# Kernel optimization log

Hardware: AMD Instinct MI355X
Metric: run time of the kernel (lower is better)

Reference implementation:

```python
import jax, jax.numpy as jnp
import numpy as np

B, S, D = 1, 2048, 4096
H = 32
Q_RANK, KV_RANK = 1536, 512
NOPE, ROPE, VD = 128, 64, 128
QD = NOPE + ROPE  # 192
EPS = 1e-6
THETA = 10000.0


def setup_inputs() -> dict:
    key = jax.random.key(0)
    ks = jax.random.split(key, 8)
    std = 0.02
    return {
        'hidden_states': jax.random.normal(ks[0], (B, S, D), jnp.float32),
        'Wq_a': jax.random.normal(ks[1], (D, Q_RANK), jnp.float32) * std,
        'q_a_ln_w': jnp.ones((Q_RANK,), jnp.float32),
        'Wq_b': jax.random.normal(ks[2], (Q_RANK, H * QD), jnp.float32) * std,
        'Wkv_a': jax.random.normal(ks[3], (D, KV_RANK + ROPE), jnp.float32) * std,
        'kv_a_ln_w': jnp.ones((KV_RANK,), jnp.float32),
        'Wkv_b': jax.random.normal(ks[4], (KV_RANK, H * (NOPE + VD)), jnp.float32) * std,
        'Wo': jax.random.normal(ks[5], (H * VD, D), jnp.float32) * std,
    }


def _rmsnorm(x, w):
    return x * jax.lax.rsqrt(jnp.mean(x * x, axis=-1, keepdims=True) + EPS) * w


def _rotate_half(x):
    h = x.shape[-1] // 2
    return jnp.concatenate([-x[..., h:], x[..., :h]], axis=-1)


def _apply_rope(x, cos, sin):
    # DeepSeek interleave permutation: view(..., d//2, 2).transpose -> [evens | odds]
    xp = jnp.concatenate([x[..., 0::2], x[..., 1::2]], axis=-1)
    return xp * cos + _rotate_half(xp) * sin


def _mla_forward(hidden_states, Wq_a, q_a_ln_w, Wq_b, Wkv_a, kv_a_ln_w, Wkv_b, Wo):
    b, s, _ = hidden_states.shape
    # low-rank query projection
    q = _rmsnorm(hidden_states @ Wq_a, q_a_ln_w) @ Wq_b          # [b,s,H*QD]
    q = q.reshape(b, s, H, QD).transpose(0, 2, 1, 3)             # [b,H,s,QD]
    q_nope, q_pe = q[..., :NOPE], q[..., NOPE:]
    # compressed kv + shared rope key
    ckv = hidden_states @ Wkv_a                                   # [b,s,KV_RANK+ROPE]
    compressed, k_pe = ckv[..., :KV_RANK], ckv[..., KV_RANK:]
    kv = _rmsnorm(compressed, kv_a_ln_w) @ Wkv_b                 # [b,s,H*(NOPE+VD)]
    kv = kv.reshape(b, s, H, NOPE + VD).transpose(0, 2, 1, 3)    # [b,H,s,NOPE+VD]
    k_nope, v = kv[..., :NOPE], kv[..., NOPE:]
    k_pe = k_pe[:, None, :, :]                                    # [b,1,s,ROPE]
    # rotary tables (cos/sin duplicated halves)
    inv_freq = 1.0 / (THETA ** (jnp.arange(0, ROPE, 2, dtype=jnp.float32) / ROPE))
    freqs = jnp.outer(jnp.arange(s, dtype=jnp.float32), inv_freq)  # [s,ROPE/2]
    emb = jnp.concatenate([freqs, freqs], axis=-1)                 # [s,ROPE]
    cos = jnp.cos(emb)[None, None].astype(hidden_states.dtype)
    sin = jnp.sin(emb)[None, None].astype(hidden_states.dtype)
    q_pe = _apply_rope(q_pe, cos, sin)
    k_pe = _apply_rope(k_pe, cos, sin)
    # assemble full q/k heads
    qf = jnp.concatenate([q_nope, q_pe], axis=-1)                 # [b,H,s,QD]
    kf = jnp.concatenate([k_nope, jnp.broadcast_to(k_pe, (b, H, s, ROPE))], axis=-1)
    scale = QD ** (-0.5)
    scores = jnp.einsum('bhqd,bhkd->bhqk', qf, kf) * scale        # [b,H,s,s]
    causal = jnp.tril(jnp.ones((s, s), dtype=bool))
    scores = jnp.where(causal, scores, jnp.finfo(scores.dtype).min)
    probs = jax.nn.softmax(scores, axis=-1)
    o = jnp.einsum('bhqk,bhkd->bhqd', probs, v)                   # [b,H,s,VD]
    o = o.transpose(0, 2, 1, 3).reshape(b, s, H * VD)
    return o @ Wo


def reference(hidden_states, Wq_a, q_a_ln_w, Wq_b, Wkv_a, kv_a_ln_w, Wkv_b, Wo):
    return _mla_forward(hidden_states, Wq_a, q_a_ln_w, Wq_b, Wkv_a, kv_a_ln_w, Wkv_b, Wo)
```

## Files before the change

### kernel.cpp

```cpp
#include <hip/hip_runtime.h>

typedef unsigned short u16;
using bf16x8 = __attribute__((ext_vector_type(8))) __bf16;
using f32x4  = __attribute__((ext_vector_type(4))) float;
using s16x8  = __attribute__((ext_vector_type(8))) short;
using s16x4  = __attribute__((ext_vector_type(4))) short;

#define AS1 __attribute__((address_space(1)))
#define AS3 __attribute__((address_space(3)))

__device__ __forceinline__ void gload16(const u16* g, u16* l) {
  __builtin_amdgcn_global_load_lds((AS1 void*)(size_t)g, (AS3 void*)l, 16, 0, 0);
}

__device__ __forceinline__ u16 f2bf(float f) {
  unsigned u = __float_as_uint(f);
  u += 0x7fffu + ((u >> 16) & 1u);
  return (u16)(u >> 16);
}
__device__ __forceinline__ float bf2f(u16 h) {
  return __uint_as_float(((unsigned)h) << 16);
}

__global__ __launch_bounds__(256) void cast_bf16_kernel(const float* __restrict__ x,
                                                        u16* __restrict__ y, int n) {
  int i = (blockIdx.x * 256 + threadIdx.x) * 4;
  if (i + 3 < n) {
    float4 v = *reinterpret_cast<const float4*>(x + i);
    s16x4 o;
    o[0] = (short)f2bf(v.x); o[1] = (short)f2bf(v.y);
    o[2] = (short)f2bf(v.z); o[3] = (short)f2bf(v.w);
    *reinterpret_cast<s16x4*>(y + i) = o;
  }
}

__global__ __launch_bounds__(256) void transpose_cast_kernel(const float* __restrict__ W,
                                                             u16* __restrict__ WT,
                                                             int K, int N) {
  __shared__ u16 tile[64][72];
  const int t = threadIdx.x;
  const int nb = blockIdx.x * 64, kb = blockIdx.y * 64;
  const int rr = t >> 3;
  const int cc = (t & 7) * 8;
#pragma unroll
  for (int pass = 0; pass < 2; ++pass) {
    const float* src = W + (size_t)(kb + pass * 32 + rr) * N + nb + cc;
    float4 a = *reinterpret_cast<const float4*>(src);
    float4 b = *reinterpret_cast<const float4*>(src + 4);
    u16* tr = &tile[pass * 32 + rr][cc];
    tr[0] = f2bf(a.x); tr[1] = f2bf(a.y); tr[2] = f2bf(a.z); tr[3] = f2bf(a.w);
    tr[4] = f2bf(b.x); tr[5] = f2bf(b.y); tr[6] = f2bf(b.z); tr[7] = f2bf(b.w);
  }
  __syncthreads();
#pragma unroll
  for (int pass = 0; pass < 2; ++pass) {
    s16x8 v;
#pragma unroll
    for (int j = 0; j < 8; ++j) v[j] = (short)tile[cc + j][pass * 32 + rr];
    *reinterpret_cast<s16x8*>(WT + (size_t)(nb + pass * 32 + rr) * K + kb + cc) = v;
  }
}

__global__ __launch_bounds__(256) void rmsnorm_kernel(const u16* __restrict__ x,
                                                      const float* __restrict__ w,
                                                      u16* __restrict__ y,
                                                      int R, int xs, int ys) {
  const int row = blockIdx.x, t = threadIdx.x;
  const u16* xr = x + (size_t)row * xs;
  float ss = 0.f;
  for (int i = t; i < R; i += 256) { float f = bf2f(xr[i]); ss += f * f; }
#pragma unroll
  for (int m = 32; m >= 1; m >>= 1) ss += __shfl_xor(ss, m);
  __shared__ float red[4];
  if ((t & 63) == 0) red[t >> 6] = ss;
  __syncthreads();
  float tot = red[0] + red[1] + red[2] + red[3];
  float r = rsqrtf(tot / (float)R + 1e-6f);
  u16* yr = y + (size_t)row * ys;
  for (int i = t; i < R; i += 256) yr[i] = f2bf(bf2f(xr[i]) * r * w[i]);
}

__global__ __launch_bounds__(256) void rope_table_kernel(float* __restrict__ cost,
                                                         float* __restrict__ sint) {
  int idx = blockIdx.x * 256 + threadIdx.x;
  int pos = idx >> 5, j = idx & 31;
  float inv = __expf(-(float)j * (9.210340371976184f / 32.0f));
  float f = (float)pos * inv;
  cost[idx] = cosf(f);
  sint[idx] = sinf(f);
}

__global__ __launch_bounds__(256) void build_qf_kernel(const u16* __restrict__ q,
                                                       const float* __restrict__ cost,
                                                       const float* __restrict__ sint,
                                                       u16* __restrict__ qf) {
  int tid = blockIdx.x * 256 + threadIdx.x;
  int o8 = tid * 8;
  if (o8 >= 32 * 2048 * 192) return;
  const float scale = 0.07216878364870323f;
  int c = (o8 % 192) >> 3;
  int rest = o8 / 192;
  int s = rest & 2047, h = rest >> 11;
  const u16* qrow = q + ((size_t)s * 32 + h) * 192;
  s16x8 out;
  if (c < 16) {
    s16x8 v = *reinterpret_cast<const s16x8*>(qrow + c * 8);
#pragma unroll
    for (int j = 0; j < 8; ++j) out[j] = (short)f2bf(bf2f((u16)v[j]) * scale);
  } else {
    int j0 = c * 8 - 128;
    bool lo = j0 < 32;
    int jj0 = lo ? j0 : j0 - 32;
    s16x8 a = *reinterpret_cast<const s16x8*>(qrow + 128 + 2 * jj0);
    s16x8 b = *reinterpret_cast<const s16x8*>(qrow + 128 + 2 * jj0 + 8);
    float4 c0 = *reinterpret_cast<const float4*>(cost + s * 32 + jj0);
    float4 c1 = *reinterpret_cast<const float4*>(cost + s * 32 + jj0 + 4);
    float4 s0 = *reinterpret_cast<const float4*>(sint + s * 32 + jj0);
    float4 s1 = *reinterpret_cast<const float4*>(sint + s * 32 + jj0 + 4);
    float cs[8] = {c0.x, c0.y, c0.z, c0.w, c1.x, c1.y, c1.z, c1.w};
    float sn[8] = {s0.x, s0.y, s0.z, s0.w, s1.x, s1.y, s1.z, s1.w};
#pragma unroll
    for (int j = 0; j < 8; ++j) {
      float x0 = bf2f((u16)((j < 4) ? a[2 * j] : b[2 * j - 8]));
      float x1 = bf2f((u16)((j < 4) ? a[2 * j + 1] : b[2 * j - 7]));
      float v = lo ? (x0 * cs[j] - x1 * sn[j]) : (x1 * cs[j] + x0 * sn[j]);
      out[j] = (short)f2bf(v * scale);
    }
  }
  *reinterpret_cast<s16x8*>(qf + o8) = out;
}

__global__ __launch_bounds__(256) void build_kf_kernel(const u16* __restrict__ kv,
                                                       const u16* __restrict__ ckv,
                                                       const float* __restrict__ cost,
                                                       const float* __restrict__ sint,
                                                       u16* __restrict__ kf) {
  int tid = blockIdx.x * 256 + threadIdx.x;
  int o8 = tid * 8;
  if (o8 >= 32 * 2048 * 192) return;
  int c = (o8 % 192) >> 3;
  int rest = o8 / 192;
  int s = rest & 2047, h = rest >> 11;
  s16x8 out;
  if (c < 16) {
    out = *reinterpret_cast<const s16x8*>(kv + ((size_t)s * 32 + h) * 256 + c * 8);
  } else {
    int j0 = c * 8 - 128;
    bool lo = j0 < 32;
    int jj0 = lo ? j0 : j0 - 32;
    const u16* crow = ckv + (size_t)s * 2112 + 512;
    s16x8 a = *reinterpret_cast<const s16x8*>(crow + 2 * jj0);
    s16x8 b = *reinterpret_cast<const s16x8*>(crow + 2 * jj0 + 8);
    float4 c0 = *reinterpret_cast<const float4*>(cost + s * 32 + jj0);
    float4 c1 = *reinterpret_cast<const float4*>(cost + s * 32 + jj0 + 4);
    float4 s0 = *reinterpret_cast<const float4*>(sint + s * 32 + jj0);
    float4 s1 = *reinterpret_cast<const float4*>(sint + s * 32 + jj0 + 4);
    float cs[8] = {c0.x, c0.y, c0.z, c0.w, c1.x, c1.y, c1.z, c1.w};
    float sn[8] = {s0.x, s0.y, s0.z, s0.w, s1.x, s1.y, s1.z, s1.w};
#pragma unroll
    for (int j = 0; j < 8; ++j) {
      float x0 = bf2f((u16)((j < 4) ? a[2 * j] : b[2 * j - 8]));
      float x1 = bf2f((u16)((j < 4) ? a[2 * j + 1] : b[2 * j - 7]));
      float v = lo ? (x0 * cs[j] - x1 * sn[j]) : (x1 * cs[j] + x0 * sn[j]);
      out[j] = (short)f2bf(v);
    }
  }
  *reinterpret_cast<s16x8*>(kf + o8) = out;
}

__global__ __launch_bounds__(256) void vt_build_kernel(const u16* __restrict__ kv,
                                                       u16* __restrict__ vT) {
  __shared__ u16 tile[64][72];
  const int t = threadIdx.x;
  const int sb = blockIdx.x * 64, db = blockIdx.y * 64, h = blockIdx.z;
  const int rr = t >> 3, cc = (t & 7) * 8;
#pragma unroll
  for (int pass = 0; pass < 2; ++pass) {
    const u16* src = kv + (size_t)(sb + pass * 32 + rr) * 8192 + h * 256 + 128 + db + cc;
    s16x8 v = *reinterpret_cast<const s16x8*>(src);
#pragma unroll
    for (int j = 0; j < 8; ++j) tile[pass * 32 + rr][cc + j] = (u16)v[j];
  }
  __syncthreads();
#pragma unroll
  for (int pass = 0; pass < 2; ++pass) {
    s16x8 v;
#pragma unroll
    for (int j = 0; j < 8; ++j) v[j] = (short)tile[cc + j][pass * 32 + rr];
    *reinterpret_cast<s16x8*>(vT + ((size_t)h * 128 + db + pass * 32 + rr) * 2048 + sb + cc) = v;
  }
}

template <int OUT_BF16>
__global__ __launch_bounds__(256) void gemm_v3_kernel(const u16* __restrict__ A,
                                                      const u16* __restrict__ BT,
                                                      void* __restrict__ Cv,
                                                      int M, int N, int K) {
  __shared__ __align__(16) u16 S[4 * 8192];
  const int t0 = threadIdx.x;
  const int lane = t0 & 63, wave = t0 >> 6;
  const int wr = wave >> 1, wc = wave & 1;
  const int row0 = blockIdx.y * 128, col0 = blockIdx.x * 128;
  const int lrow = lane & 15, lkg = lane >> 4;

  const int lp = lane ^ ((lane >> 3) & 3);
  const int srow_off = lp >> 2;
  const int skel = (lp & 3) * 8;
  const int c0 = wave * 2, c1 = c0 + 1;
  const int arow_c0 = row0 + c0 * 16 + srow_off;
  const int arow_c1 = row0 + c1 * 16 + srow_off;
  int brow_c0 = col0 + c0 * 16 + srow_off; if (brow_c0 > N - 1) brow_c0 = N - 1;
  int brow_c1 = col0 + c1 * 16 + srow_off; if (brow_c1 > N - 1) brow_c1 = N - 1;

  int aoff[4], boff[4];
#pragma unroll
  for (int m = 0; m < 4; ++m) {
    int r = wr * 64 + m * 16 + lrow;
    int off = r * 32 + lkg * 8;
    aoff[m] = off ^ ((off >> 3) & 0x18);
    r = wc * 64 + m * 16 + lrow;
    off = r * 32 + lkg * 8;
    boff[m] = off ^ ((off >> 3) & 0x18);
  }

  const int NT = K >> 5;

#pragma unroll
  for (int pt = 0; pt < 3; ++pt) {
    u16* ab = &S[pt * 8192];
    const int kb = pt * 32 + skel;
    gload16(A  + (size_t)arow_c0 * K + kb, ab + c0 * 512);
    gload16(A  + (size_t)arow_c1 * K + kb, ab + c1 * 512);
    gload16(BT + (size_t)brow_c0 * K + kb, ab + 4096 + c0 * 512);
    gload16(BT + (size_t)brow_c1 * K + kb, ab + 4096 + c1 * 512);
  }

  f32x4 acc[4][4];
#pragma unroll
  for (int m = 0; m < 4; ++m)
#pragma unroll
    for (int n = 0; n < 4; ++n) acc[m][n] = 0.f;

  for (int t = 0; t < NT; ++t) {
    if (t + 2 < NT)      asm volatile("s_waitcnt vmcnt(8)" ::: "memory");
    else if (t + 1 < NT) asm volatile("s_waitcnt vmcnt(4)" ::: "memory");
    else                 asm volatile("s_waitcnt vmcnt(0)" ::: "memory");
    __builtin_amdgcn_s_barrier();
    __builtin_amdgcn_sched_barrier(0);

    const u16* ab = &S[(t & 3) * 8192];
    bf16x8 af[4], bb[4];
#pragma unroll
    for (int m = 0; m < 4; ++m)
      af[m] = *reinterpret_cast<const bf16x8*>(ab + aoff[m]);
#pragma unroll
    for (int n = 0; n < 4; ++n)
      bb[n] = *reinterpret_cast<const bf16x8*>(ab + 4096 + boff[n]);

    if (t + 3 < NT) {
      u16* sb = &S[((t + 3) & 3) * 8192];
      const int kb = (t + 3) * 32 + skel;
      gload16(A  + (size_t)arow_c0 * K + kb, sb + c0 * 512);
      gload16(A  + (size_t)arow_c1 * K + kb, sb + c1 * 512);
      gload16(BT + (size_t)brow_c0 * K + kb, sb + 4096 + c0 * 512);
      gload16(BT + (size_t)brow_c1 * K + kb, sb + 4096 + c1 * 512);
    }

    __builtin_amdgcn_s_setprio(1);
#pragma unroll
    for (int m = 0; m < 4; ++m)
#pragma unroll
      for (int n = 0; n < 4; ++n)
        acc[m][n] = __builtin_amdgcn_mfma_f32_16x16x32_bf16(af[m], bb[n], acc[m][n], 0, 0, 0);
    __builtin_amdgcn_s_setprio(0);
  }

#pragma unroll
  for (int m = 0; m < 4; ++m) {
#pragma unroll
    for (int n = 0; n < 4; ++n) {
      int col = col0 + wc * 64 + n * 16 + lrow;
      if (col < N) {
#pragma unroll
        for (int i = 0; i < 4; ++i) {
          int row = row0 + wr * 64 + m * 16 + lkg * 4 + i;
          size_t idx = (size_t)row * N + col;
          if (OUT_BF16) ((u16*)Cv)[idx] = f2bf(acc[m][n][i]);
          else          ((float*)Cv)[idx] = acc[m][n][i];
        }
      }
    }
  }
}

__global__ __launch_bounds__(256) void mla_attn_kernel(const u16* __restrict__ qf,
                                                       const u16* __restrict__ kf,
                                                       const u16* __restrict__ vT,
                                                       u16* __restrict__ o) {
  const int h = blockIdx.x, pair = blockIdx.y;
  const int t = threadIdx.x, wave = t >> 6, lane = t & 63;
  const int lrow = lane & 15, lkg = lane >> 4;
  __shared__ __align__(16) u16 Kt[24 * 512];
  __shared__ __align__(16) u16 Vt[16 * 512];
  __shared__ __align__(16) u16 Pl[4][16][72];

  const u16* ksrc0 = kf + ((size_t)h * 2048 + wave * 16 + lrow) * 192 + lkg * 8;
  const u16* vsrc0 = vT + ((size_t)h * 128 + wave * 32 + lrow) * 2048 + lkg * 8;

  for (int qq = 0; qq < 2; ++qq) {
    const int qb = qq ? (31 - pair) : pair;
    const int qbase = qb * 64 + wave * 16;

    bf16x8 qfr[6];
    const u16* qrow_ptr = qf + ((size_t)h * 2048 + qbase + lrow) * 192;
#pragma unroll
    for (int kk = 0; kk < 6; ++kk)
      qfr[kk] = *reinterpret_cast<const bf16x8*>(qrow_ptr + kk * 32 + lkg * 8);

    f32x4 acc_o[8];
#pragma unroll
    for (int f = 0; f < 8; ++f) acc_o[f] = 0.f;
    float m_run[4], l_run[4];
#pragma unroll
    for (int i = 0; i < 4; ++i) { m_run[i] = -__builtin_inff(); l_run[i] = 0.f; }

    const int kv_end = qb * 64 + 64;
    for (int kt = 0; kt < kv_end; kt += 64) {
      {
        const u16* ks = ksrc0 + (size_t)kt * 192;
#pragma unroll
        for (int kk = 0; kk < 6; ++kk)
          gload16(ks + kk * 32, &Kt[(wave * 6 + kk) * 512]);
#pragma unroll
        for (int j = 0; j < 4; ++j) {
          int fo = (j >> 1), ck = j & 1;
          gload16(vsrc0 + (size_t)fo * 16 * 2048 + kt + ck * 32,
                  &Vt[((wave * 2 + fo) * 2 + ck) * 512]);
        }
      }
      __syncthreads();

      f32x4 sv[4];
#pragma unroll
      for (int cg = 0; cg < 4; ++cg) sv[cg] = 0.f;
#pragma unroll
      for (int cg = 0; cg < 4; ++cg)
#pragma unroll
        for (int kk = 0; kk < 6; ++kk) {
          bf16x8 kfr = *reinterpret_cast<const bf16x8*>(&Kt[(cg * 6 + kk) * 512 + lane * 8]);
          sv[cg] = __builtin_amdgcn_mfma_f32_16x16x32_bf16(qfr[kk], kfr, sv[cg], 0, 0, 0);
        }

      const int qrow_b = qbase + lkg * 4;
      if (kt + 64 >= kv_end) {
#pragma unroll
        for (int cg = 0; cg < 4; ++cg) {
          int kvcol = kt + cg * 16 + lrow;
#pragma unroll
          for (int i = 0; i < 4; ++i)
            if (kvcol > qrow_b + i) sv[cg][i] = -__builtin_inff();
        }
      }
      float tmax[4], m_new[4], alpha[4], rsum[4], p[4][4];
#pragma unroll
      for (int i = 0; i < 4; ++i)
        tmax[i] = fmaxf(fmaxf(sv[0][i], sv[1][i]), fmaxf(sv[2][i], sv[3][i]));
#pragma unroll
      for (int m = 8; m >= 1; m >>= 1)
#pragma unroll
        for (int i = 0; i < 4; ++i) tmax[i] = fmaxf(tmax[i], __shfl_xor(tmax[i], m));
#pragma unroll
      for (int i = 0; i < 4; ++i) {
        m_new[i] = fmaxf(m_run[i], tmax[i]);
#pragma unroll
        for (int cg = 0; cg < 4; ++cg) p[cg][i] = __expf(sv[cg][i] - m_new[i]);
        rsum[i] = (p[0][i] + p[1][i]) + (p[2][i] + p[3][i]);
      }
#pragma unroll
      for (int m = 8; m >= 1; m >>= 1)
#pragma unroll
        for (int i = 0; i < 4; ++i) rsum[i] += __shfl_xor(rsum[i], m);
#pragma unroll
      for (int i = 0; i < 4; ++i) {
        alpha[i] = __expf(m_run[i] - m_new[i]);
        l_run[i] = l_run[i] * alpha[i] + rsum[i];
        m_run[i] = m_new[i];
      }
#pragma unroll
      for (int f = 0; f < 8; ++f)
#pragma unroll
        for (int i = 0; i < 4; ++i) acc_o[f][i] *= alpha[i];
#pragma unroll
      for (int cg = 0; cg < 4; ++cg)
#pragma unroll
        for (int i = 0; i < 4; ++i)
          Pl[wave][lkg * 4 + i][cg * 16 + lrow] = f2bf(p[cg][i]);
#pragma unroll
      for (int ck = 0; ck < 2; ++ck) {
        bf16x8 pf = *reinterpret_cast<const bf16x8*>(&Pl[wave][lrow][ck * 32 + lkg * 8]);
#pragma unroll
        for (int f = 0; f < 8; ++f) {
          bf16x8 vfr = *reinterpret_cast<const bf16x8*>(&Vt[(f * 2 + ck) * 512 + lane * 8]);
          acc_o[f] = __builtin_amdgcn_mfma_f32_16x16x32_bf16(pf, vfr, acc_o[f], 0, 0, 0);
        }
      }
      __syncthreads();
    }
#pragma unroll
    for (int f = 0; f < 8; ++f)
#pragma unroll
      for (int i = 0; i < 4; ++i) {
        int row = qbase + lkg * 4 + i;
        int col = h * 128 + f * 16 + lrow;
        o[(size_t)row * 4096 + col] = f2bf(acc_o[f][i] / l_run[i]);
      }
  }
}

extern "C" void kernel_launch(void* const* d_in, const int* in_sizes, int n_in,
                              void* d_out, int out_size, void* d_ws, size_t ws_size,
                              hipStream_t stream) {
  (void)in_sizes; (void)n_in; (void)out_size; (void)ws_size;
  const float* hs   = (const float*)d_in[0];
  const float* Wqa  = (const float*)d_in[1];
  const float* qln  = (const float*)d_in[2];
  const float* Wqb  = (const float*)d_in[3];
  const float* Wkva = (const float*)d_in[4];
  const float* kvln = (const float*)d_in[5];
  const float* Wkvb = (const float*)d_in[6];
  const float* Wo   = (const float*)d_in[7];
  float* out = (float*)d_out;

  char* p = (char*)d_ws;
  size_t off = 0;
  auto carve = [&](size_t bytes) {
    char* r = p + off;
    off += (bytes + 255) & ~(size_t)255;
    return r;
  };
  u16* hs_bf = (u16*)carve((size_t)2048 * 4096 * 2);
  u16* WabT  = (u16*)carve((size_t)2112 * 4096 * 2);
  u16* WqbT  = (u16*)carve((size_t)6144 * 1536 * 2);
  u16* WkvbT = (u16*)carve((size_t)8192 * 512 * 2);
  u16* WoT   = (u16*)carve((size_t)4096 * 4096 * 2);
  u16* fused = (u16*)carve((size_t)2048 * 2112 * 2);
  u16* qan   = (u16*)carve((size_t)2048 * 1536 * 2);
  u16* q     = (u16*)carve((size_t)2048 * 6144 * 2);
  u16* cn    = (u16*)carve((size_t)2048 * 512 * 2);
  u16* kv    = (u16*)carve((size_t)2048 * 8192 * 2);
  u16* qfb   = (u16*)carve((size_t)32 * 2048 * 192 * 2);
  u16* kfb   = (u16*)carve((size_t)32 * 2048 * 192 * 2);
  u16* vTb   = (u16*)carve((size_t)32 * 128 * 2048 * 2);
  u16* ob    = (u16*)carve((size_t)2048 * 4096 * 2);
  float* cost = (float*)carve((size_t)65536 * 4);
  float* sint = (float*)carve((size_t)65536 * 4);

  cast_bf16_kernel<<<8192, 256, 0, stream>>>(hs, hs_bf, 2048 * 4096);
  transpose_cast_kernel<<<dim3(24, 64), 256, 0, stream>>>(Wqa, WabT, 4096, 1536);
  transpose_cast_kernel<<<dim3(9, 64), 256, 0, stream>>>(Wkva, WabT + (size_t)1536 * 4096, 4096, 576);
  transpose_cast_kernel<<<dim3(96, 24), 256, 0, stream>>>(Wqb, WqbT, 1536, 6144);
  transpose_cast_kernel<<<dim3(128, 8), 256, 0, stream>>>(Wkvb, WkvbT, 512, 8192);
  transpose_cast_kernel<<<dim3(64, 64), 256, 0, stream>>>(Wo, WoT, 4096, 4096);
  rope_table_kernel<<<256, 256, 0, stream>>>(cost, sint);

  gemm_v3_kernel<1><<<dim3(17, 16), 256, 0, stream>>>(hs_bf, WabT, fused, 2048, 2112, 4096);

  rmsnorm_kernel<<<2048, 256, 0, stream>>>(fused, qln, qan, 1536, 2112, 1536);
  rmsnorm_kernel<<<2048, 256, 0, stream>>>(fused + 1536, kvln, cn, 512, 2112, 512);

  gemm_v3_kernel<1><<<dim3(48, 16), 256, 0, stream>>>(qan, WqbT, q, 2048, 6144, 1536);
  gemm_v3_kernel<1><<<dim3(64, 16), 256, 0, stream>>>(cn, WkvbT, kv, 2048, 8192, 512);

  build_qf_kernel<<<6144, 256, 0, stream>>>(q, cost, sint, qfb);
  build_kf_kernel<<<6144, 256, 0, stream>>>(kv, fused + 1536, cost, sint, kfb);
  vt_build_kernel<<<dim3(32, 2, 32), 256, 0, stream>>>(kv, vTb);

  mla_attn_kernel<<<dim3(32, 16), 256, 0, stream>>>(qfb, kfb, vTb, ob);

  gemm_v3_kernel<0><<<dim3(32, 16), 256, 0, stream>>>(ob, WoT, out, 2048, 4096, 4096);
}
```

Before: 430.2 us.

## Restructure attention into 2-wave blocks, each wave owning 32 query rows

```diff
diff --git a/kernel.cpp b/kernel.cpp
--- a/kernel.cpp
+++ b/kernel.cpp
@@ -293,128 +293,158 @@
   }
 }
 
-__global__ __launch_bounds__(256) void mla_attn_kernel(const u16* __restrict__ qf,
+__global__ __launch_bounds__(128) void mla_attn_kernel(const u16* __restrict__ qf,
                                                        const u16* __restrict__ kf,
                                                        const u16* __restrict__ vT,
                                                        u16* __restrict__ o) {
-  const int h = blockIdx.x, pair = blockIdx.y;
+  const int h = blockIdx.x, qb = 31 - blockIdx.y;
   const int t = threadIdx.x, wave = t >> 6, lane = t & 63;
   const int lrow = lane & 15, lkg = lane >> 4;
   __shared__ __align__(16) u16 Kt[24 * 512];
   __shared__ __align__(16) u16 Vt[16 * 512];
-  __shared__ __align__(16) u16 Pl[4][16][72];
-
-  const u16* ksrc0 = kf + ((size_t)h * 2048 + wave * 16 + lrow) * 192 + lkg * 8;
-  const u16* vsrc0 = vT + ((size_t)h * 128 + wave * 32 + lrow) * 2048 + lkg * 8;
-
-  for (int qq = 0; qq < 2; ++qq) {
-    const int qb = qq ? (31 - pair) : pair;
-    const int qbase = qb * 64 + wave * 16;
-
-    bf16x8 qfr[6];
-    const u16* qrow_ptr = qf + ((size_t)h * 2048 + qbase + lrow) * 192;
+  __shared__ __align__(16) u16 Pl[2][32][72];
+
+  const u16* ksrcA = kf + ((size_t)h * 2048 + (2 * wave) * 16 + lrow) * 192 + lkg * 8;
+  const u16* ksrcB = ksrcA + (size_t)16 * 192;
+  const u16* vsrc0 = vT + ((size_t)h * 128 + (4 * wave) * 16 + lrow) * 2048 + lkg * 8;
+
+  const int qbase = qb * 64 + wave * 32;
+
+  bf16x8 qfr[2][6];
+#pragma unroll
+  for (int r = 0; r < 2; ++r) {
+    const u16* qp = qf + ((size_t)h * 2048 + qbase + r * 16 + lrow) * 192 + lkg * 8;
 #pragma unroll
     for (int kk = 0; kk < 6; ++kk)
-      qfr[kk] = *reinterpret_cast<const bf16x8*>(qrow_ptr + kk * 32 + lkg * 8);
-
-    f32x4 acc_o[8];
-#pragma unroll
-    for (int f = 0; f < 8; ++f) acc_o[f] = 0.f;
-    float m_run[4], l_run[4];
-#pragma unroll
-    for (int i = 0; i < 4; ++i) { m_run[i] = -__builtin_inff(); l_run[i] = 0.f; }
-
-    const int kv_end = qb * 64 + 64;
-    for (int kt = 0; kt < kv_end; kt += 64) {
-      {
-        const u16* ks = ksrc0 + (size_t)kt * 192;
-#pragma unroll
-        for (int kk = 0; kk < 6; ++kk)
-          gload16(ks + kk * 32, &Kt[(wave * 6 + kk) * 512]);
-#pragma unroll
-        for (int j = 0; j < 4; ++j) {
-          int fo = (j >> 1), ck = j & 1;
-          gload16(vsrc0 + (size_t)fo * 16 * 2048 + kt + ck * 32,
-                  &Vt[((wave * 2 + fo) * 2 + ck) * 512]);
-        }
-      }
-      __syncthreads();
-
-      f32x4 sv[4];
-#pragma unroll
-      for (int cg = 0; cg < 4; ++cg) sv[cg] = 0.f;
-#pragma unroll
-      for (int cg = 0; cg < 4; ++cg)
-#pragma unroll
-        for (int kk = 0; kk < 6; ++kk) {
-          bf16x8 kfr = *reinterpret_cast<const bf16x8*>(&Kt[(cg * 6 + kk) * 512 + lane * 8]);
-          sv[cg] = __builtin_amdgcn_mfma_f32_16x16x32_bf16(qfr[kk], kfr, sv[cg], 0, 0, 0);
-        }
-
-      const int qrow_b = qbase + lkg * 4;
-      if (kt + 64 >= kv_end) {
+      qfr[r][kk] = *reinterpret_cast<const bf16x8*>(qp + kk * 32);
+  }
+
+  f32x4 acc[2][8];
+#pragma unroll
+  for (int r = 0; r < 2; ++r)
+#pragma unroll
+    for (int f = 0; f < 8; ++f) acc[r][f] = 0.f;
+  float m_run[2][4], l_par[2][4];
+#pragma unroll
+  for (int r = 0; r < 2; ++r)
+#pragma unroll
+    for (int i = 0; i < 4; ++i) { m_run[r][i] = -1e30f; l_par[r][i] = 0.f; }
+
+  const int kv_end = qb * 64 + 64;
+  for (int kt = 0; kt < kv_end; kt += 64) {
+    {
+      const u16* ka = ksrcA + (size_t)kt * 192;
+      const u16* kb = ksrcB + (size_t)kt * 192;
+#pragma unroll
+      for (int kk = 0; kk < 6; ++kk) {
+        gload16(ka + kk * 32, &Kt[((2 * wave) * 6 + kk) * 512]);
+        gload16(kb + kk * 32, &Kt[((2 * wave + 1) * 6 + kk) * 512]);
+      }
+#pragma unroll
+      for (int j = 0; j < 4; ++j) {
+#pragma unroll
+        for (int ck = 0; ck < 2; ++ck)
+          gload16(vsrc0 + (size_t)j * 16 * 2048 + kt + ck * 32,
+                  &Vt[((4 * wave + j) * 2 + ck) * 512]);
+      }
+    }
+    __syncthreads();
+
+    f32x4 sv[2][4];
+#pragma unroll
+    for (int r = 0; r < 2; ++r)
+#pragma unroll
+      for (int cg = 0; cg < 4; ++cg) sv[r][cg] = 0.f;
+#pragma unroll
+    for (int cg = 0; cg < 4; ++cg)
+#pragma unroll
+      for (int kk = 0; kk < 6; ++kk) {
+        bf16x8 kfr = *reinterpret_cast<const bf16x8*>(&Kt[(cg * 6 + kk) * 512 + lane * 8]);
+        sv[0][cg] = __builtin_amdgcn_mfma_f32_16x16x32_bf16(qfr[0][kk], kfr, sv[0][cg], 0, 0, 0);
+        sv[1][cg] = __builtin_amdgcn_mfma_f32_16x16x32_bf16(qfr[1][kk], kfr, sv[1][cg], 0, 0, 0);
+      }
+
+    if (kt + 64 >= kv_end) {
+#pragma unroll
+      for (int r = 0; r < 2; ++r)
 #pragma unroll
         for (int cg = 0; cg < 4; ++cg) {
           int kvcol = kt + cg * 16 + lrow;
+          int rowb = qbase + r * 16 + lkg * 4;
 #pragma unroll
           for (int i = 0; i < 4; ++i)
-            if (kvcol > qrow_b + i) sv[cg][i] = -__builtin_inff();
+            if (kvcol > rowb + i) sv[r][cg][i] = -__builtin_inff();
         }
-      }
-      float tmax[4], m_new[4], alpha[4], rsum[4], p[4][4];
+    }
+
+#pragma unroll
+    for (int r = 0; r < 2; ++r) {
+      float tmax[4];
 #pragma unroll
       for (int i = 0; i < 4; ++i)
-        tmax[i] = fmaxf(fmaxf(sv[0][i], sv[1][i]), fmaxf(sv[2][i], sv[3][i]));
+        tmax[i] = fmaxf(fmaxf(sv[r][0][i], sv[r][1][i]), fmaxf(sv[r][2][i], sv[r][3][i]));
 #pragma unroll
       for (int m = 8; m >= 1; m >>= 1)
 #pragma unroll
         for (int i = 0; i < 4; ++i) tmax[i] = fmaxf(tmax[i], __shfl_xor(tmax[i], m));
+      int need = 0;
+#pragma unroll
+      for (int i = 0; i < 4; ++i) need |= (tmax[i] > m_run[r][i] + 8.f) ? 1 : 0;
+      if (__any(need)) {
+#pragma unroll
+        for (int i = 0; i < 4; ++i) {
+          float mnew = fmaxf(m_run[r][i], tmax[i]);
+          float alpha = __expf(m_run[r][i] - mnew);
+          m_run[r][i] = mnew;
+          l_par[r][i] *= alpha;
+#pragma unroll
+          for (int f = 0; f < 8; ++f) acc[r][f][i] *= alpha;
+        }
+      }
 #pragma unroll
       for (int i = 0; i < 4; ++i) {
-        m_new[i] = fmaxf(m_run[i], tmax[i]);
-#pragma unroll
-        for (int cg = 0; cg < 4; ++cg) p[cg][i] = __expf(sv[cg][i] - m_new[i]);
-        rsum[i] = (p[0][i] + p[1][i]) + (p[2][i] + p[3][i]);
-      }
-#pragma unroll
-      for (int m = 8; m >= 1; m >>= 1)
-#pragma unroll
-        for (int i = 0; i < 4; ++i) rsum[i] += __shfl_xor(rsum[i], m);
+#pragma unroll
+        for (int cg = 0; cg < 4; ++cg) sv[r][cg][i] = __expf(sv[r][cg][i] - m_run[r][i]);
+        l_par[r][i] += (sv[r][0][i] + sv[r][1][i]) + (sv[r][2][i] + sv[r][3][i]);
+      }
+#pragma unroll
+      for (int cg = 0; cg < 4; ++cg)
+#pragma unroll
+        for (int i = 0; i < 4; ++i)
+          Pl[wave][r * 16 + lkg * 4 + i][cg * 16 + lrow] = f2bf(sv[r][cg][i]);
+    }
+
+#pragma unroll
+    for (int ck = 0; ck < 2; ++ck) {
+      bf16x8 pf0 = *reinterpret_cast<const bf16x8*>(&Pl[wave][lrow][ck * 32 + lkg * 8]);
+      bf16x8 pf1 = *reinterpret_cast<const bf16x8*>(&Pl[wave][16 + lrow][ck * 32 + lkg * 8]);
+#pragma unroll
+      for (int f = 0; f < 8; ++f) {
+        bf16x8 vfr = *reinterpret_cast<const bf16x8*>(&Vt[(f * 2 + ck) * 512 + lane * 8]);
+        acc[0][f] = __builtin_amdgcn_mfma_f32_16x16x32_bf16(pf0, vfr, acc[0][f], 0, 0, 0);
+        acc[1][f] = __builtin_amdgcn_mfma_f32_16x16x32_bf16(pf1, vfr, acc[1][f], 0, 0, 0);
+      }
+    }
+    __syncthreads();
+  }
+
+#pragma unroll
+  for (int r = 0; r < 2; ++r)
+#pragma unroll
+    for (int i = 0; i < 4; ++i) {
+#pragma unroll
+      for (int m = 8; m >= 1; m >>= 1) l_par[r][i] += __shfl_xor(l_par[r][i], m);
+    }
+#pragma unroll
+  for (int r = 0; r < 2; ++r)
+#pragma unroll
+    for (int f = 0; f < 8; ++f)
 #pragma unroll
       for (int i = 0; i < 4; ++i) {
-        alpha[i] = __expf(m_run[i] - m_new[i]);
-        l_run[i] = l_run[i] * alpha[i] + rsum[i];
-        m_run[i] = m_new[i];
-      }
-#pragma unroll
-      for (int f = 0; f < 8; ++f)
-#pragma unroll
-        for (int i = 0; i < 4; ++i) acc_o[f][i] *= alpha[i];
-#pragma unroll
-      for (int cg = 0; cg < 4; ++cg)
-#pragma unroll
-        for (int i = 0; i < 4; ++i)
-          Pl[wave][lkg * 4 + i][cg * 16 + lrow] = f2bf(p[cg][i]);
-#pragma unroll
-      for (int ck = 0; ck < 2; ++ck) {
-        bf16x8 pf = *reinterpret_cast<const bf16x8*>(&Pl[wave][lrow][ck * 32 + lkg * 8]);
-#pragma unroll
-        for (int f = 0; f < 8; ++f) {
-          bf16x8 vfr = *reinterpret_cast<const bf16x8*>(&Vt[(f * 2 + ck) * 512 + lane * 8]);
-          acc_o[f] = __builtin_amdgcn_mfma_f32_16x16x32_bf16(pf, vfr, acc_o[f], 0, 0, 0);
-        }
-      }
-      __syncthreads();
-    }
-#pragma unroll
-    for (int f = 0; f < 8; ++f)
-#pragma unroll
-      for (int i = 0; i < 4; ++i) {
-        int row = qbase + lkg * 4 + i;
+        int row = qbase + r * 16 + lkg * 4 + i;
         int col = h * 128 + f * 16 + lrow;
-        o[(size_t)row * 4096 + col] = f2bf(acc_o[f][i] / l_run[i]);
-      }
-  }
+        o[(size_t)row * 4096 + col] = f2bf(acc[r][f][i] / l_par[r][i]);
+      }
 }
 
 extern "C" void kernel_launch(void* const* d_in, const int* in_sizes, int n_in,
@@ -475,7 +505,7 @@
   build_kf_kernel<<<6144, 256, 0, stream>>>(kv, fused + 1536, cost, sint, kfb);
   vt_build_kernel<<<dim3(32, 2, 32), 256, 0, stream>>>(kv, vTb);
 
-  mla_attn_kernel<<<dim3(32, 16), 256, 0, stream>>>(qfb, kfb, vTb, ob);
+  mla_attn_kernel<<<dim3(32, 32), 128, 0, stream>>>(qfb, kfb, vTb, ob);
 
   gemm_v3_kernel<0><<<dim3(32, 16), 256, 0, stream>>>(ob, WoT, out, 2048, 4096, 4096);
 }
```

New measurement: 457.7 us. 1.06x slower.
